# Kernel tuning notes

Hardware: AMD Instinct MI355X
Metric: run time of the kernel (lower is better)

Reference implementation:

```python
import jax, jax.numpy as jnp
import numpy as np

N_NODES = 1_000_000
DIM = 128
L = 80        # walk length
L_NS = 10     # negative samples
BATCH = 8192


def setup_inputs() -> dict:
    key = jax.random.key(0)
    k1, k2 = jax.random.split(key)
    # kaiming_normal_ on [n_nodes, dim]: std = sqrt(2 / fan_in) with fan_in = dim
    X = jax.random.normal(k1, (N_NODES, DIM), dtype=jnp.float32) * np.sqrt(2.0 / DIM)
    rw_batch = jax.random.randint(k2, (BATCH, L + 1 + L_NS), 0, N_NODES, dtype=jnp.int64)
    return {"X": X, "rw_batch": rw_batch, "l": L}


def reference(X, rw_batch, l):
    # X: [n_nodes, dim]; rw_batch: [B, l+1+l_ns] int indices
    X_start = X[rw_batch[:, 0]]                    # [B, d]
    X_all = X[rw_batch]                            # [B, l+1+l_ns, d] (gather)
    # scores[b, k] = <X[rw_batch[b, k]], X_start[b]>
    scores = jnp.einsum('bkd,bd->bk', X_all, X_start)   # [B, l+1+l_ns]
    # numerator: sum of dots with walk nodes 1..l
    numerator = jnp.sum(scores[:, 1:l + 1], axis=1)      # [B]
    # denominator: all walk columns (unique(dim=1) is a no-op modulo column order
    # for distinct random columns; the sum is permutation-invariant) + negatives
    denom = jnp.log(jnp.sum(jnp.exp(scores), axis=1))    # [B]
    loss = l * denom - numerator
    return jnp.mean(loss)
```

## Files before the change

### kernel.cpp

```cpp
#include <hip/hip_runtime.h>
#include <math.h>

#define BATCH 8192
#define WALK  91
#define LVAL  80
#define DIM   128
#define ROWS_PER_BLOCK 4

__global__ __launch_bounds__(256, 8)
void node2vec_loss_kernel(const float* __restrict__ X,
                          const int* __restrict__ rw,
                          float* __restrict__ row_loss) {
    __shared__ int s_idx[ROWS_PER_BLOCK * WALK];

    const int wave = threadIdx.x >> 6;
    const int lane = threadIdx.x & 63;
    const int row_base = blockIdx.x * ROWS_PER_BLOCK;

    for (int i = threadIdx.x; i < ROWS_PER_BLOCK * WALK; i += 256) {
        s_idx[i] = rw[row_base * WALK + i];
    }
    __syncthreads();

    const int* my_idx = s_idx + wave * WALK;
    const int b = row_base + wave;

    const long long idx0 = (long long)my_idx[0];
    const float2 xs = *(const float2*)(X + idx0 * DIM + lane * 2);

    float sumexp = 0.0f;
    float num = 0.0f;

    for (int k0 = 0; k0 < WALK; k0 += 7) {
        float2 v[7];
        #pragma unroll
        for (int j = 0; j < 7; ++j) {
            const long long idx = (long long)my_idx[k0 + j];
            v[j] = *(const float2*)(X + idx * DIM + lane * 2);
        }
        #pragma unroll
        for (int j = 0; j < 7; ++j) {
            float p = v[j].x * xs.x + v[j].y * xs.y;
            p += __shfl_xor(p, 1);
            p += __shfl_xor(p, 2);
            p += __shfl_xor(p, 4);
            p += __shfl_xor(p, 8);
            p += __shfl_xor(p, 16);
            p += __shfl_xor(p, 32);
            sumexp += expf(p);
            const int k = k0 + j;
            if (k >= 1 && k <= LVAL) num += p;
        }
    }

    if (lane == 0) {
        row_loss[b] = (float)LVAL * logf(sumexp) - num;
    }
}

__global__ __launch_bounds__(256)
void reduce_mean_kernel(const float* __restrict__ row_loss,
                        float* __restrict__ out) {
    __shared__ double sdata[256];
    double acc = 0.0;
    for (int i = threadIdx.x; i < BATCH; i += 256) {
        acc += (double)row_loss[i];
    }
    sdata[threadIdx.x] = acc;
    __syncthreads();
    for (int s = 128; s > 0; s >>= 1) {
        if ((int)threadIdx.x < s) sdata[threadIdx.x] += sdata[threadIdx.x + s];
        __syncthreads();
    }
    if (threadIdx.x == 0) {
        out[0] = (float)(sdata[0] / (double)BATCH);
    }
}

extern "C" void kernel_launch(void* const* d_in, const int* in_sizes, int n_in,
                              void* d_out, int out_size, void* d_ws, size_t ws_size,
                              hipStream_t stream) {
    const float* X = (const float*)d_in[0];
    const int* rw = (const int*)d_in[1];
    float* row_loss = (float*)d_ws;
    float* out = (float*)d_out;

    node2vec_loss_kernel<<<BATCH / ROWS_PER_BLOCK, 256, 0, stream>>>(X, rw, row_loss);
    reduce_mean_kernel<<<1, 256, 0, stream>>>(row_loss, out);
}
```

Measured before the change: 74.42 us.

## Split each wave into four 16-lane groups processing separate walk rows

Each wave now splits into four 16-lane groups, and each group handles a different walk column per iteration. Each lane loads 8 floats as two float4 instead of one float2, so a 64-lane dot product becomes a 16-lane one with four shuffle steps instead of six. The partial sums are combined across groups at the end. It also switches to the fast __expf/__logf intrinsics, trading some accuracy for cheaper transcendentals. The last iteration pads by clamping its index to 0 and masking the result.

```diff
diff --git a/kernel.cpp b/kernel.cpp
--- a/kernel.cpp
+++ b/kernel.cpp
@@ -15,6 +15,8 @@
 
     const int wave = threadIdx.x >> 6;
     const int lane = threadIdx.x & 63;
+    const int grp  = lane >> 4;
+    const int sub  = lane & 15;
     const int row_base = blockIdx.x * ROWS_PER_BLOCK;
 
     for (int i = threadIdx.x; i < ROWS_PER_BLOCK * WALK; i += 256) {
@@ -25,36 +27,42 @@
     const int* my_idx = s_idx + wave * WALK;
     const int b = row_base + wave;
 
-    const long long idx0 = (long long)my_idx[0];
-    const float2 xs = *(const float2*)(X + idx0 * DIM + lane * 2);
+    const size_t idx0 = (size_t)my_idx[0];
+    const float4 xs0 = *(const float4*)(X + idx0 * DIM + sub * 8);
+    const float4 xs1 = *(const float4*)(X + idx0 * DIM + sub * 8 + 4);
 
     float sumexp = 0.0f;
-    float num = 0.0f;
+    float num    = 0.0f;
 
-    for (int k0 = 0; k0 < WALK; k0 += 7) {
-        float2 v[7];
-        #pragma unroll
-        for (int j = 0; j < 7; ++j) {
-            const long long idx = (long long)my_idx[k0 + j];
-            v[j] = *(const float2*)(X + idx * DIM + lane * 2);
-        }
-        #pragma unroll
-        for (int j = 0; j < 7; ++j) {
-            float p = v[j].x * xs.x + v[j].y * xs.y;
-            p += __shfl_xor(p, 1);
-            p += __shfl_xor(p, 2);
-            p += __shfl_xor(p, 4);
-            p += __shfl_xor(p, 8);
-            p += __shfl_xor(p, 16);
-            p += __shfl_xor(p, 32);
-            sumexp += expf(p);
-            const int k = k0 + j;
+    #pragma unroll 4
+    for (int i = 0; i < 23; ++i) {
+        const int k = i * 4 + grp;
+        const int kc = (k < WALK) ? k : 0;
+        const size_t idx = (size_t)my_idx[kc];
+        const float4* base = (const float4*)(X + idx * DIM + sub * 8);
+        const float4 a = base[0];
+        const float4 c = base[1];
+
+        float p = a.x * xs0.x + a.y * xs0.y + a.z * xs0.z + a.w * xs0.w
+                + c.x * xs1.x + c.y * xs1.y + c.z * xs1.z + c.w * xs1.w;
+        p += __shfl_xor(p, 1);
+        p += __shfl_xor(p, 2);
+        p += __shfl_xor(p, 4);
+        p += __shfl_xor(p, 8);
+
+        if (k < WALK) {
+            sumexp += __expf(p);
             if (k >= 1 && k <= LVAL) num += p;
         }
     }
 
+    sumexp += __shfl_xor(sumexp, 16);
+    sumexp += __shfl_xor(sumexp, 32);
+    num    += __shfl_xor(num, 16);
+    num    += __shfl_xor(num, 32);
+
     if (lane == 0) {
-        row_loss[b] = (float)LVAL * logf(sumexp) - num;
+        row_loss[b] = (float)LVAL * __logf(sumexp) - num;
     }
 }
 
```

Result: faster. 71.26 us (-4.2%).
